# Performance work log

Hardware: AMD Instinct MI355X
Metric: run time of the kernel (lower is better)

## Reference

```python
import jax, jax.numpy as jnp
import numpy as np

# Module hyperparameters (from init_kwargs)
START = 0.0      # lower distance cutoff
STOP = 5.0       # radius_graph cutoff r
K = 32           # max_num_neighbors
N_ATOMS = 16384
N_GRAPHS = 64
BOX = 30.0       # box edge length (Angstrom) -> realistic density for r=5 cutoff


def setup_inputs() -> dict:
    key = jax.random.key(0)
    k1, k2 = jax.random.split(key)
    pos = jax.random.uniform(k1, (N_ATOMS, 3), dtype=jnp.float32) * BOX
    batch = jnp.sort(jax.random.randint(k2, (N_ATOMS,), 0, N_GRAPHS)).astype(jnp.int64)
    return {"pos": pos, "batch": batch}


def reference(pos, batch):
    """radius_graph (loop=False) + edge vectors/norms + lower-cutoff mask.

    Because jit requires static shapes, the variable-length edge list of the
    original is returned in padded form: edge_index [2, N*K], edge_weight [N*K],
    edge_vec [N*K, 3], plus a boolean validity mask [N*K]. Valid entries match
    the original (edge_index, edge_weight, edge_vec) after compaction.
    """
    N = pos.shape[0]
    # Pairwise squared distances via the Gram trick: [N, N], memory-bound.
    sq = jnp.sum(pos * pos, axis=-1)
    d2 = sq[:, None] + sq[None, :] - 2.0 * (pos @ pos.T)
    idx = jnp.arange(N)
    valid = (batch[:, None] == batch[None, :]) \
            & (idx[:, None] != idx[None, :]) \
            & (d2 <= STOP * STOP)
    d2m = jnp.where(valid, d2, jnp.inf)
    # Up to K nearest neighbors within the radius per node.
    neg_d2, nbr = jax.lax.top_k(-d2m, K)          # [N, K]
    nbr_valid = neg_d2 > -jnp.inf                  # in-radius, same-graph, non-self
    nbr = jnp.where(nbr_valid, nbr, idx[:, None])  # pad with self (vec = 0)
    # edge_vec = pos[center] - pos[neighbor]  (pos[edge_index[0]] - pos[edge_index[1]])
    edge_vec = pos[:, None, :] - pos[nbr]          # [N, K, 3]
    sqd = jnp.sum(edge_vec * edge_vec, axis=-1)
    w = jnp.where(nbr_valid, jnp.sqrt(jnp.where(nbr_valid, sqd, 1.0)), 0.0)
    lower = nbr_valid & (w >= START)               # lower cutoff mask
    src = jnp.broadcast_to(idx[:, None], (N, K))
    edge_index = jnp.stack([src.reshape(-1), nbr.reshape(-1)])  # [2, N*K]
    mask = lower.reshape(-1)
    edge_weight = jnp.where(lower, w, 0.0).reshape(-1)
    edge_vec = jnp.where(lower[..., None], edge_vec, 0.0).reshape(-1, 3)
    return edge_index, edge_weight, edge_vec, mask
```

## Files before the change

### kernel.cpp

```cpp
#include <hip/hip_runtime.h>
#include <math.h>

#define KNBR 32
#define STOP2 25.0
#define BAND 1.0e-3f
#define CAND_CAP 1024
#define CAP 64
#define WPB 8

__global__ __launch_bounds__(WPB * 64)
void radius_graph_knn(const float* __restrict__ pos,
                      const int* __restrict__ batch,
                      float* __restrict__ out, int n) {
    __shared__ float spos[3 * CAND_CAP];
    __shared__ int   sbatch[CAND_CAP];
    __shared__ int   jbuf[WPB][CAP];
    __shared__ int   win[WPB][KNBR];

    const int tid  = threadIdx.x;
    const int lane = tid & 63;
    const int w    = tid >> 6;
    const int i0   = blockIdx.x * WPB;
    const int i    = min(i0 + w, n - 1);

    const int bFirst = batch[i0];
    const int bLast  = batch[min(i0 + WPB - 1, n - 1)];
    const int nchunks = (n + 63) >> 6;
    const int c0 = i0 >> 6;
    const int cw = c0 - 32 + lane;
    bool rel = false;
    if (cw >= 0 && cw < nchunks) {
        const int s = batch[cw << 6];
        const int e = batch[min(n - 1, (cw << 6) + 63)];
        rel = (s <= bLast) && (e >= bFirst);
    }
    const unsigned long long cm = __ballot(rel);
    const int cLo = c0 - 32 + (int)__builtin_ctzll(cm);
    const int cHi = c0 - 32 + (63 - (int)__builtin_clzll(cm));
    const int base = cLo << 6;
    int stagedN = min(n, (cHi + 1) << 6) - base;
    if (stagedN > CAND_CAP) stagedN = CAND_CAP;

    {
        const float4* __restrict__ src = (const float4*)(pos + 3 * (size_t)base);
        float4* __restrict__ dst = (float4*)spos;
        const int nvec = (3 * stagedN) >> 2;
        for (int t = tid; t < nvec; t += WPB * 64) dst[t] = src[t];
        for (int t = tid; t < stagedN; t += WPB * 64) sbatch[t] = batch[base + t];
    }
    __syncthreads();

    const int si = i - base;
    const float xi = spos[3 * si], yi = spos[3 * si + 1], zi = spos[3 * si + 2];
    const int b = sbatch[si];
    const double xid = xi, yid = yi, zid = zi;

    int count = 0;
    for (int t0 = 0; t0 < stagedN; t0 += 64) {
        const int t = t0 + lane;
        const int tc = min(t, stagedN - 1);
        const float xj = spos[3 * tc], yj = spos[3 * tc + 1], zj = spos[3 * tc + 2];
        const int bj = sbatch[tc];
        const float dx = xi - xj, dy = yi - yj, dz = zi - zj;
        const float d2 = dx * dx + dy * dy + dz * dz;
        const int j = base + tc;
        const bool valid = (t < stagedN) & (j != i) & (bj == b) &
                           (d2 <= 25.0f + BAND);
        const unsigned long long m = __ballot(valid);
        const int p = count + __popcll(m & ((1ULL << lane) - 1ULL));
        if (valid && p < CAP) jbuf[w][p] = tc;
        count += __popcll(m);
    }
    if (count > CAP) count = CAP;

    double d2e = 1e300;
    int jmine = 0x7fffffff, slot = 0;
    bool valid = false;
    if (lane < count) {
        slot = jbuf[w][lane];
        const double dx = xid - (double)spos[3 * slot];
        const double dy = yid - (double)spos[3 * slot + 1];
        const double dz = zid - (double)spos[3 * slot + 2];
        d2e = dx * dx + dy * dy + dz * dz;
        jmine = base + slot;
        valid = (d2e <= STOP2);
    }
    const unsigned long long vm = __ballot(valid);
    int nsel = __popcll(vm);
    if (nsel > KNBR) nsel = KNBR;
    int rank = 0;
    for (int s = 0; s < count; ++s) {
        const double ds = __shfl(d2e, s);
        const int    js = __shfl(jmine, s);
        const bool   vs = (vm >> s) & 1ULL;
        rank += (vs && (ds < d2e || (ds == d2e && js < jmine))) ? 1 : 0;
    }
    if (valid && rank < KNBR) win[w][rank] = slot;

    const long long NK = (long long)n * KNBR;
    float* row0 = out;
    float* row1 = out + NK;
    float* wgt  = out + 2 * NK;
    float* vec  = out + 3 * NK;
    float* msk  = out + 6 * NK;
    const long long obase = (long long)i * KNBR;

    if ((i0 + w) < n && lane < KNBR) {
        const int s = lane;
        const bool v = (s < nsel);
        const int sl = v ? win[w][s] : si;
        const int j = base + sl;
        const float vx = xi - spos[3 * sl];
        const float vy = yi - spos[3 * sl + 1];
        const float vz = zi - spos[3 * sl + 2];
        const float ww = v ? sqrtf(vx * vx + vy * vy + vz * vz) : 0.0f;
        row0[obase + s] = (float)i;
        row1[obase + s] = (float)j;
        wgt[obase + s]  = ww;
        vec[3 * (obase + s) + 0] = v ? vx : 0.0f;
        vec[3 * (obase + s) + 1] = v ? vy : 0.0f;
        vec[3 * (obase + s) + 2] = v ? vz : 0.0f;
        msk[obase + s]  = v ? 1.0f : 0.0f;
    }
}

extern "C" void kernel_launch(void* const* d_in, const int* in_sizes, int n_in,
                              void* d_out, int out_size, void* d_ws, size_t ws_size,
                              hipStream_t stream) {
    const float* pos   = (const float*)d_in[0];
    const int*   batch = (const int*)d_in[1];
    float* out = (float*)d_out;
    int n = in_sizes[1];

    const int block = WPB * 64;
    const int grid = (n + WPB * 64 - 1) / (WPB * 64) * 64;
    radius_graph_knn<<<(n + WPB - 1) / WPB, block, 0, stream>>>(pos, batch, out, n);
}
```

Before: 70.09 us.

## Process two atoms per wavefront to amortize candidate staging and loads

Each wavefront now handles two center atoms instead of one, so a block covers 16 atoms and the grid is halved. The shared-memory staging of positions and batch ids is amortized over twice as many atoms. In the candidate scan, each candidate position read from LDS is reused for both atoms. Selection and output are then done one atom after the other, which adds per-wave serial work and register pressure in exchange for fewer blocks and less redundant staging.

```diff
diff --git a/kernel.cpp b/kernel.cpp
--- a/kernel.cpp
+++ b/kernel.cpp
@@ -7,6 +7,8 @@
 #define CAND_CAP 1024
 #define CAP 64
 #define WPB 8
+#define APW 2
+#define APB (WPB*APW)
 
 __global__ __launch_bounds__(WPB * 64)
 void radius_graph_knn(const float* __restrict__ pos,
@@ -14,17 +16,16 @@
                       float* __restrict__ out, int n) {
     __shared__ float spos[3 * CAND_CAP];
     __shared__ int   sbatch[CAND_CAP];
-    __shared__ int   jbuf[WPB][CAP];
+    __shared__ int   jbuf[WPB][APW][CAP];
     __shared__ int   win[WPB][KNBR];
 
     const int tid  = threadIdx.x;
     const int lane = tid & 63;
     const int w    = tid >> 6;
-    const int i0   = blockIdx.x * WPB;
-    const int i    = min(i0 + w, n - 1);
+    const int i0   = blockIdx.x * APB;
 
     const int bFirst = batch[i0];
-    const int bLast  = batch[min(i0 + WPB - 1, n - 1)];
+    const int bLast  = batch[min(i0 + APB - 1, n - 1)];
     const int nchunks = (n + 63) >> 6;
     const int c0 = i0 >> 6;
     const int cw = c0 - 32 + lane;
@@ -50,52 +51,36 @@
     }
     __syncthreads();
 
-    const int si = i - base;
-    const float xi = spos[3 * si], yi = spos[3 * si + 1], zi = spos[3 * si + 2];
-    const int b = sbatch[si];
-    const double xid = xi, yid = yi, zid = zi;
+    int ia[APW]; int ba[APW];
+    float xa[APW], ya[APW], za[APW];
+    #pragma unroll
+    for (int a = 0; a < APW; ++a) {
+        const int i = min(i0 + w * APW + a, n - 1);
+        ia[a] = i;
+        const int si = i - base;
+        xa[a] = spos[3 * si]; ya[a] = spos[3 * si + 1]; za[a] = spos[3 * si + 2];
+        ba[a] = sbatch[si];
+    }
 
-    int count = 0;
+    int cnt[APW] = {0, 0};
     for (int t0 = 0; t0 < stagedN; t0 += 64) {
         const int t = t0 + lane;
         const int tc = min(t, stagedN - 1);
         const float xj = spos[3 * tc], yj = spos[3 * tc + 1], zj = spos[3 * tc + 2];
         const int bj = sbatch[tc];
-        const float dx = xi - xj, dy = yi - yj, dz = zi - zj;
-        const float d2 = dx * dx + dy * dy + dz * dz;
         const int j = base + tc;
-        const bool valid = (t < stagedN) & (j != i) & (bj == b) &
-                           (d2 <= 25.0f + BAND);
-        const unsigned long long m = __ballot(valid);
-        const int p = count + __popcll(m & ((1ULL << lane) - 1ULL));
-        if (valid && p < CAP) jbuf[w][p] = tc;
-        count += __popcll(m);
+        #pragma unroll
+        for (int a = 0; a < APW; ++a) {
+            const float dx = xa[a] - xj, dy = ya[a] - yj, dz = za[a] - zj;
+            const float d2 = dx * dx + dy * dy + dz * dz;
+            const bool valid = (t < stagedN) & (j != ia[a]) & (bj == ba[a]) &
+                               (d2 <= 25.0f + BAND);
+            const unsigned long long m = __ballot(valid);
+            const int p = cnt[a] + __popcll(m & ((1ULL << lane) - 1ULL));
+            if (valid && p < CAP) jbuf[w][a][p] = tc;
+            cnt[a] += __popcll(m);
+        }
     }
-    if (count > CAP) count = CAP;
-
-    double d2e = 1e300;
-    int jmine = 0x7fffffff, slot = 0;
-    bool valid = false;
-    if (lane < count) {
-        slot = jbuf[w][lane];
-        const double dx = xid - (double)spos[3 * slot];
-        const double dy = yid - (double)spos[3 * slot + 1];
-        const double dz = zid - (double)spos[3 * slot + 2];
-        d2e = dx * dx + dy * dy + dz * dz;
-        jmine = base + slot;
-        valid = (d2e <= STOP2);
-    }
-    const unsigned long long vm = __ballot(valid);
-    int nsel = __popcll(vm);
-    if (nsel > KNBR) nsel = KNBR;
-    int rank = 0;
-    for (int s = 0; s < count; ++s) {
-        const double ds = __shfl(d2e, s);
-        const int    js = __shfl(jmine, s);
-        const bool   vs = (vm >> s) & 1ULL;
-        rank += (vs && (ds < d2e || (ds == d2e && js < jmine))) ? 1 : 0;
-    }
-    if (valid && rank < KNBR) win[w][rank] = slot;
 
     const long long NK = (long long)n * KNBR;
     float* row0 = out;
@@ -103,24 +88,53 @@
     float* wgt  = out + 2 * NK;
     float* vec  = out + 3 * NK;
     float* msk  = out + 6 * NK;
-    const long long obase = (long long)i * KNBR;
 
-    if ((i0 + w) < n && lane < KNBR) {
-        const int s = lane;
-        const bool v = (s < nsel);
-        const int sl = v ? win[w][s] : si;
-        const int j = base + sl;
-        const float vx = xi - spos[3 * sl];
-        const float vy = yi - spos[3 * sl + 1];
-        const float vz = zi - spos[3 * sl + 2];
-        const float ww = v ? sqrtf(vx * vx + vy * vy + vz * vz) : 0.0f;
-        row0[obase + s] = (float)i;
-        row1[obase + s] = (float)j;
-        wgt[obase + s]  = ww;
-        vec[3 * (obase + s) + 0] = v ? vx : 0.0f;
-        vec[3 * (obase + s) + 1] = v ? vy : 0.0f;
-        vec[3 * (obase + s) + 2] = v ? vz : 0.0f;
-        msk[obase + s]  = v ? 1.0f : 0.0f;
+    #pragma unroll
+    for (int a = 0; a < APW; ++a) {
+        const int count = min(cnt[a], CAP);
+        double d2e = 1e300;
+        int jmine = 0x7fffffff, slot = 0;
+        bool valid = false;
+        if (lane < count) {
+            slot = jbuf[w][a][lane];
+            const double dx = (double)xa[a] - (double)spos[3 * slot];
+            const double dy = (double)ya[a] - (double)spos[3 * slot + 1];
+            const double dz = (double)za[a] - (double)spos[3 * slot + 2];
+            d2e = dx * dx + dy * dy + dz * dz;
+            jmine = base + slot;
+            valid = (d2e <= STOP2);
+        }
+        const unsigned long long vm = __ballot(valid);
+        int nsel = __popcll(vm);
+        if (nsel > KNBR) nsel = KNBR;
+        int rank = 0;
+        for (int s = 0; s < count; ++s) {
+            const double ds = __shfl(d2e, s);
+            const int    js = __shfl(jmine, s);
+            const bool   vs = (vm >> s) & 1ULL;
+            rank += (vs && (ds < d2e || (ds == d2e && js < jmine))) ? 1 : 0;
+        }
+        if (valid && rank < KNBR) win[w][rank] = slot;
+
+        const int i = ia[a];
+        const long long obase = (long long)i * KNBR;
+        if (lane < KNBR) {
+            const int s = lane;
+            const bool v = (s < nsel);
+            const int sl = v ? win[w][s] : (i - base);
+            const int j = base + sl;
+            const float vx = xa[a] - spos[3 * sl];
+            const float vy = ya[a] - spos[3 * sl + 1];
+            const float vz = za[a] - spos[3 * sl + 2];
+            const float ww = v ? sqrtf(vx * vx + vy * vy + vz * vz) : 0.0f;
+            row0[obase + s] = (float)i;
+            row1[obase + s] = (float)j;
+            wgt[obase + s]  = ww;
+            vec[3 * (obase + s) + 0] = v ? vx : 0.0f;
+            vec[3 * (obase + s) + 1] = v ? vy : 0.0f;
+            vec[3 * (obase + s) + 2] = v ? vz : 0.0f;
+            msk[obase + s]  = v ? 1.0f : 0.0f;
+        }
     }
 }
 
@@ -133,6 +147,6 @@
     int n = in_sizes[1];
 
     const int block = WPB * 64;
-    const int grid = (n + WPB * 64 - 1) / (WPB * 64) * 64;
-    radius_graph_knn<<<(n + WPB - 1) / WPB, block, 0, stream>>>(pos, batch, out, n);
+    const int grid = (n + APB - 1) / APB;
+    radius_graph_knn<<<grid, block, 0, stream>>>(pos, batch, out, n);
 }
```

Measured after the change: 69.00 us. Within noise of the previous version (-1.5%).
